# Kernel tuning notes

Measured on AMD Instinct MI355X. Metric: run time of the kernel, lower is better.

Reference implementation:

```python
import jax, jax.numpy as jnp
import numpy as np

NV, P, C, H, O = 50000, 32, 4, 64, 128
EPS = 1e-5


def _bn(x, g, b, m, v):
    # inference-mode BatchNorm1d over channel dim
    return (x - m) * jax.lax.rsqrt(v + EPS) * g + b


def setup_inputs() -> dict:
    key = jax.random.key(0)
    ks = jax.random.split(key, 16)
    voxel_features = jax.random.normal(ks[0], (NV, P, C), jnp.float32)
    voxel_num_points = jax.random.randint(ks[1], (NV,), 1, P + 1).astype(jnp.int64)
    def lin(k, fin, fout):
        kw, kb = jax.random.split(k)
        s = 1.0 / np.sqrt(fin)
        W = jax.random.uniform(kw, (fin, fout), jnp.float32, -s, s)
        b = jax.random.uniform(kb, (fout,), jnp.float32, -s, s)
        return W, b
    W1, b1 = lin(ks[2], C, H)
    W2, b2 = lin(ks[3], H, H)
    W3, b3 = lin(ks[4], H, O)
    g1 = jax.random.uniform(ks[5], (H,), jnp.float32, 0.5, 1.5)
    be1 = jax.random.normal(ks[6], (H,), jnp.float32) * 0.1
    m1 = jax.random.normal(ks[7], (H,), jnp.float32) * 0.1
    v1 = jax.random.uniform(ks[8], (H,), jnp.float32, 0.5, 1.5)
    g2 = jax.random.uniform(ks[9], (H,), jnp.float32, 0.5, 1.5)
    be2 = jax.random.normal(ks[10], (H,), jnp.float32) * 0.1
    m2 = jax.random.normal(ks[11], (H,), jnp.float32) * 0.1
    v2 = jax.random.uniform(ks[12], (H,), jnp.float32, 0.5, 1.5)
    return dict(voxel_features=voxel_features, voxel_num_points=voxel_num_points,
                W1=W1, b1=b1, g1=g1, be1=be1, m1=m1, v1=v1,
                W2=W2, b2=b2, g2=g2, be2=be2, m2=m2, v2=v2,
                W3=W3, b3=b3)


def reference(voxel_features, voxel_num_points,
              W1, b1, g1, be1, m1, v1,
              W2, b2, g2, be2, m2, v2,
              W3, b3):
    nv, p, c = voxel_features.shape
    x = voxel_features.reshape(-1, c)                 # (NV*P, C)
    x = jax.nn.relu(_bn(x @ W1 + b1, g1, be1, m1, v1))
    x = jax.nn.relu(_bn(x @ W2 + b2, g2, be2, m2, v2))
    x = x @ W3 + b3                                   # (NV*P, O)
    x = x.reshape(nv, p, -1)
    mask = jnp.arange(p)[None, :] < voxel_num_points[:, None]  # (NV, P)
    # original multiplies by mask then masked-fills -inf; net effect is -inf fill
    x = jnp.where(mask[:, :, None], x, -jnp.inf)
    return jnp.max(x, axis=1)                         # (NV, O)
```

## Files before the change

kernel.cpp:

```cpp
#include <hip/hip_runtime.h>
#include <math.h>

#define NVOX 50000
#define PPTS 32
#define HDIM 64
#define ODIM 128
#define EPSBN 1e-5f

typedef _Float16 f16x8 __attribute__((ext_vector_type(8)));
typedef _Float16 f16x4 __attribute__((ext_vector_type(4)));
typedef float f32x4 __attribute__((ext_vector_type(4)));

#define LO4(v) __builtin_shufflevector(v, v, 0, 1, 2, 3)
#define HI4(v) __builtin_shufflevector(v, v, 4, 5, 6, 7)

#define WS_W1C 0
#define WS_W2T 512
#define WS_W3T 4608
#define WS_F32_BYTE 25600
#define FOLD_THREADS 12992

__global__ void vfe_fold(
    const float* __restrict__ W1, const float* __restrict__ b1,
    const float* __restrict__ g1, const float* __restrict__ be1,
    const float* __restrict__ m1, const float* __restrict__ v1,
    const float* __restrict__ W2, const float* __restrict__ b2,
    const float* __restrict__ g2, const float* __restrict__ be2,
    const float* __restrict__ m2, const float* __restrict__ v2,
    const float* __restrict__ W3, const float* __restrict__ b3,
    _Float16* __restrict__ wsh, float* __restrict__ wsf)
{
    int t = blockIdx.x * 256 + threadIdx.x;
    if (t < 512) {
        int row = t >> 3, i = t & 7;
        float s1 = g1[row] * rsqrtf(v1[row] + EPSBN);
        float val;
        if (i < 4)      val = W1[i * 64 + row] * s1;
        else if (i == 4) val = (b1[row] - m1[row]) * s1 + be1[row];
        else             val = 0.f;
        wsh[WS_W1C + t] = (_Float16)val;
    } else if (t < 4608) {
        int e = t - 512;
        int chp = e >> 6;
        int rem = e & 63;
        int qq = rem >> 4, kc = (rem >> 2) & 3, j = rem & 3;
        int ch = kc * 16 + qq * 4 + j;
        float s2 = g2[chp] * rsqrtf(v2[chp] + EPSBN);
        wsh[t] = (_Float16)(W2[ch * 64 + chp] * s2);
    } else if (t < 12800) {
        int e = t - 4608;
        int o = e >> 6;
        int rem = e & 63;
        int php = rem >> 3, j8 = rem & 7;
        int gl = php ^ (o & 7);
        int idx = gl * 8 + j8;
        int qq = idx >> 4, kc = (idx >> 2) & 3, j = idx & 3;
        int ch = kc * 16 + qq * 4 + j;
        wsh[t] = (_Float16)W3[ch * 128 + o];
    } else if (t < 12864) {
        int i = t - 12800;
        float s2 = g2[i] * rsqrtf(v2[i] + EPSBN);
        wsf[i] = (b2[i] - m2[i]) * s2 + be2[i];
    } else if (t < FOLD_THREADS) {
        int i = t - 12864;
        wsf[64 + i] = b3[i];
    }
}

static __device__ __forceinline__ f16x4 relu4(f32x4 a) {
    f16x4 h;
    h[0] = (_Float16)fmaxf(a[0], 0.f);
    h[1] = (_Float16)fmaxf(a[1], 0.f);
    h[2] = (_Float16)fmaxf(a[2], 0.f);
    h[3] = (_Float16)fmaxf(a[3], 0.f);
    return h;
}

__global__ __launch_bounds__(256, 3) void vfe_mfma(
    const float* __restrict__ vf, const int* __restrict__ vnp,
    const _Float16* __restrict__ wsh, const float* __restrict__ wsf,
    float* __restrict__ out)
{
    __shared__ __align__(16) _Float16 sW3[ODIM * HDIM];

    const int tid  = threadIdx.x;
    const int wave = tid >> 6;
    const int lane = tid & 63;
    const int q    = lane >> 4;
    const int m16  = lane & 15;
    (void)wave;

    const int wavebase = blockIdx.x * 256 + (tid >> 6) * 64;
    const int voxA = wavebase >> 5;

    {
        const f16x8* src = (const f16x8*)&wsh[WS_W3T];
        f16x8* dst = (f16x8*)sW3;
#pragma unroll
        for (int i = 0; i < 4; ++i) dst[tid + 256 * i] = src[tid + 256 * i];
    }

    const int nA = vnp[voxA];
    const int nB = vnp[voxA + 1];

    f16x4 a1[4];
#pragma unroll
    for (int mt = 0; mt < 4; ++mt)
        a1[mt] = (q < 2) ? *(const f16x4*)&wsh[WS_W1C + (16 * mt + m16) * 8 + q * 4]
                         : (f16x4)0;
    f16x8 a2p[4][2];
#pragma unroll
    for (int mt = 0; mt < 4; ++mt)
#pragma unroll
        for (int h = 0; h < 2; ++h)
            a2p[mt][h] = *(const f16x8*)&wsh[WS_W2T + (16 * mt + m16) * 64 + q * 16 + h * 8];
    f32x4 c2v[4];
#pragma unroll
    for (int mt = 0; mt < 4; ++mt)
        c2v[mt] = *(const f32x4*)(wsf + mt * 16 + q * 4);
    float b3r[8];
#pragma unroll
    for (int nt = 0; nt < 8; ++nt) b3r[nt] = wsf[64 + nt * 16 + m16];

    float4 xv[4];
#pragma unroll
    for (int g = 0; g < 4; ++g)
        xv[g] = *(const float4*)(vf + ((size_t)wavebase + g * 16 + m16) * 4);

    f16x4 bf[4];
#pragma unroll
    for (int g = 0; g < 4; ++g) {
        f16x4 b = (f16x4)0;
        if (q == 0) {
            b[0] = (_Float16)xv[g].x; b[1] = (_Float16)xv[g].y;
            b[2] = (_Float16)xv[g].z; b[3] = (_Float16)xv[g].w;
        } else if (q == 1) {
            b[0] = (_Float16)1.0f;
        }
        bf[g] = b;
    }

    __syncthreads();

    f16x4 d1[4][4];
#pragma unroll
    for (int g = 0; g < 4; ++g)
#pragma unroll
        for (int mt = 0; mt < 4; ++mt) {
            f32x4 acc = {0.f, 0.f, 0.f, 0.f};
            acc = __builtin_amdgcn_mfma_f32_16x16x16f16(a1[mt], bf[g], acc, 0, 0, 0);
            d1[g][mt] = relu4(acc);
        }

    f16x4 d2[4][4];
#pragma unroll
    for (int g = 0; g < 4; ++g)
#pragma unroll
        for (int mt = 0; mt < 4; ++mt) {
            f32x4 acc = c2v[mt];
            acc = __builtin_amdgcn_mfma_f32_16x16x16f16(LO4(a2p[mt][0]), d1[g][0], acc, 0, 0, 0);
            acc = __builtin_amdgcn_mfma_f32_16x16x16f16(HI4(a2p[mt][0]), d1[g][1], acc, 0, 0, 0);
            acc = __builtin_amdgcn_mfma_f32_16x16x16f16(LO4(a2p[mt][1]), d1[g][2], acc, 0, 0, 0);
            acc = __builtin_amdgcn_mfma_f32_16x16x16f16(HI4(a2p[mt][1]), d1[g][3], acc, 0, 0, 0);
            d2[g][mt] = relu4(acc);
        }

    f32x4 macc4[4];
#pragma unroll
    for (int g = 0; g < 4; ++g) {
        const int n = (g < 2) ? nA : nB;
        const int slotbase = (g & 1) * 16 + q * 4;
#pragma unroll
        for (int r = 0; r < 4; ++r)
            macc4[g][r] = (slotbase + r < n) ? 0.f : -INFINITY;
    }

    float vmA[8], vmB[8];
#pragma unroll
    for (int nt = 0; nt < 8; ++nt) { vmA[nt] = -INFINITY; vmB[nt] = -INFINITY; }

#pragma unroll
    for (int nt = 0; nt < 8; ++nt) {
        const int o = nt * 16 + m16;
        f16x8 p0 = *(const f16x8*)&sW3[o * 64 + ((2 * q + 0) ^ (m16 & 7)) * 8];
        f16x8 p1 = *(const f16x8*)&sW3[o * 64 + ((2 * q + 1) ^ (m16 & 7)) * 8];
#pragma unroll
        for (int g = 0; g < 4; ++g) {
            f32x4 acc = macc4[g];
            acc = __builtin_amdgcn_mfma_f32_16x16x16f16(d2[g][0], LO4(p0), acc, 0, 0, 0);
            acc = __builtin_amdgcn_mfma_f32_16x16x16f16(d2[g][1], HI4(p0), acc, 0, 0, 0);
            acc = __builtin_amdgcn_mfma_f32_16x16x16f16(d2[g][2], LO4(p1), acc, 0, 0, 0);
            acc = __builtin_amdgcn_mfma_f32_16x16x16f16(d2[g][3], HI4(p1), acc, 0, 0, 0);
            float m0 = fmaxf(fmaxf(acc[0], acc[1]), fmaxf(acc[2], acc[3]));
            if (g < 2) vmA[nt] = fmaxf(vmA[nt], m0);
            else       vmB[nt] = fmaxf(vmB[nt], m0);
        }
    }

#pragma unroll
    for (int nt = 0; nt < 8; ++nt) {
        float t0 = vmA[nt];
        t0 = fmaxf(t0, __shfl_xor(t0, 16));
        t0 = fmaxf(t0, __shfl_xor(t0, 32));
        float t1 = vmB[nt];
        t1 = fmaxf(t1, __shfl_xor(t1, 16));
        t1 = fmaxf(t1, __shfl_xor(t1, 32));
        if (q == 0) out[(size_t)(voxA + 0) * ODIM + nt * 16 + m16] = t0 + b3r[nt];
        if (q == 1) out[(size_t)(voxA + 1) * ODIM + nt * 16 + m16] = t1 + b3r[nt];
    }
}

extern "C" void kernel_launch(void* const* d_in, const int* in_sizes, int n_in,
                              void* d_out, int out_size, void* d_ws, size_t ws_size,
                              hipStream_t stream) {
    const float* vf  = (const float*)d_in[0];
    const int*   vnp = (const int*)d_in[1];
    const float* W1  = (const float*)d_in[2];
    const float* b1  = (const float*)d_in[3];
    const float* g1  = (const float*)d_in[4];
    const float* be1 = (const float*)d_in[5];
    const float* m1  = (const float*)d_in[6];
    const float* v1  = (const float*)d_in[7];
    const float* W2  = (const float*)d_in[8];
    const float* b2  = (const float*)d_in[9];
    const float* g2  = (const float*)d_in[10];
    const float* be2 = (const float*)d_in[11];
    const float* m2  = (const float*)d_in[12];
    const float* v2  = (const float*)d_in[13];
    const float* W3  = (const float*)d_in[14];
    const float* b3  = (const float*)d_in[15];
    float* out = (float*)d_out;

    _Float16* wsh = (_Float16*)d_ws;
    float*    wsf = (float*)((char*)d_ws + WS_F32_BYTE);

    vfe_fold<<<(FOLD_THREADS + 255) / 256, 256, 0, stream>>>(
        W1, b1, g1, be1, m1, v1, W2, b2, g2, be2, m2, v2, W3, b3, wsh, wsf);

    const int blocks = (NVOX * PPTS) / 256;
    vfe_mfma<<<blocks, 256, 0, stream>>>(vf, vnp, wsh, wsf, out);
}
```

Baseline: 168.3 us.

## Process one voxel per wave, use packed f16 conversion, raise occupancy bound

Each wave now handles one voxel (32 points) instead of two, which halves the per-wave register arrays for the intermediate activations and accumulators. The launch bound is raised to 4 blocks per CU, and the grid doubles to NVOX/4 blocks. ReLU-to-f16 conversion now uses packed round-toward-zero conversion instructions instead of four scalar casts. The trade-off is that each block still copies the full W3 tile into LDS and loads all per-wave weights, so that fixed cost is paid twice as often per voxel. The conversion rounding also changes from round-to-nearest to round-toward-zero.

```diff
diff --git a/kernel.cpp b/kernel.cpp
--- a/kernel.cpp
+++ b/kernel.cpp
@@ -9,6 +9,7 @@
 
 typedef _Float16 f16x8 __attribute__((ext_vector_type(8)));
 typedef _Float16 f16x4 __attribute__((ext_vector_type(4)));
+typedef _Float16 f16x2 __attribute__((ext_vector_type(2)));
 typedef float f32x4 __attribute__((ext_vector_type(4)));
 
 #define LO4(v) __builtin_shufflevector(v, v, 0, 1, 2, 3)
@@ -68,15 +69,14 @@
 }
 
 static __device__ __forceinline__ f16x4 relu4(f32x4 a) {
-    f16x4 h;
-    h[0] = (_Float16)fmaxf(a[0], 0.f);
-    h[1] = (_Float16)fmaxf(a[1], 0.f);
-    h[2] = (_Float16)fmaxf(a[2], 0.f);
-    h[3] = (_Float16)fmaxf(a[3], 0.f);
-    return h;
-}
-
-__global__ __launch_bounds__(256, 3) void vfe_mfma(
+    f16x2 lo = __builtin_bit_cast(f16x2,
+        __builtin_amdgcn_cvt_pkrtz(fmaxf(a[0], 0.f), fmaxf(a[1], 0.f)));
+    f16x2 hi = __builtin_bit_cast(f16x2,
+        __builtin_amdgcn_cvt_pkrtz(fmaxf(a[2], 0.f), fmaxf(a[3], 0.f)));
+    return __builtin_shufflevector(lo, hi, 0, 1, 2, 3);
+}
+
+__global__ __launch_bounds__(256, 4) void vfe_mfma(
     const float* __restrict__ vf, const int* __restrict__ vnp,
     const _Float16* __restrict__ wsh, const float* __restrict__ wsf,
     float* __restrict__ out)
@@ -84,14 +84,11 @@
     __shared__ __align__(16) _Float16 sW3[ODIM * HDIM];
 
     const int tid  = threadIdx.x;
-    const int wave = tid >> 6;
     const int lane = tid & 63;
     const int q    = lane >> 4;
     const int m16  = lane & 15;
-    (void)wave;
-
-    const int wavebase = blockIdx.x * 256 + (tid >> 6) * 64;
-    const int voxA = wavebase >> 5;
+
+    const int vox = blockIdx.x * 4 + (tid >> 6);
 
     {
         const f16x8* src = (const f16x8*)&wsh[WS_W3T];
@@ -100,8 +97,7 @@
         for (int i = 0; i < 4; ++i) dst[tid + 256 * i] = src[tid + 256 * i];
     }
 
-    const int nA = vnp[voxA];
-    const int nB = vnp[voxA + 1];
+    const int n = vnp[vox];
 
     f16x4 a1[4];
 #pragma unroll
@@ -122,14 +118,14 @@
 #pragma unroll
     for (int nt = 0; nt < 8; ++nt) b3r[nt] = wsf[64 + nt * 16 + m16];
 
-    float4 xv[4];
-#pragma unroll
-    for (int g = 0; g < 4; ++g)
-        xv[g] = *(const float4*)(vf + ((size_t)wavebase + g * 16 + m16) * 4);
-
-    f16x4 bf[4];
-#pragma unroll
-    for (int g = 0; g < 4; ++g) {
+    float4 xv[2];
+#pragma unroll
+    for (int g = 0; g < 2; ++g)
+        xv[g] = *(const float4*)(vf + ((size_t)vox * 32 + g * 16 + m16) * 4);
+
+    f16x4 bf[2];
+#pragma unroll
+    for (int g = 0; g < 2; ++g) {
         f16x4 b = (f16x4)0;
         if (q == 0) {
             b[0] = (_Float16)xv[g].x; b[1] = (_Float16)xv[g].y;
@@ -142,9 +138,9 @@
 
     __syncthreads();
 
-    f16x4 d1[4][4];
-#pragma unroll
-    for (int g = 0; g < 4; ++g)
+    f16x4 d1[2][4];
+#pragma unroll
+    for (int g = 0; g < 2; ++g)
 #pragma unroll
         for (int mt = 0; mt < 4; ++mt) {
             f32x4 acc = {0.f, 0.f, 0.f, 0.f};
@@ -152,9 +148,9 @@
             d1[g][mt] = relu4(acc);
         }
 
-    f16x4 d2[4][4];
-#pragma unroll
-    for (int g = 0; g < 4; ++g)
+    f16x4 d2[2][4];
+#pragma unroll
+    for (int g = 0; g < 2; ++g)
 #pragma unroll
         for (int mt = 0; mt < 4; ++mt) {
             f32x4 acc = c2v[mt];
@@ -165,19 +161,18 @@
             d2[g][mt] = relu4(acc);
         }
 
-    f32x4 macc4[4];
-#pragma unroll
-    for (int g = 0; g < 4; ++g) {
-        const int n = (g < 2) ? nA : nB;
-        const int slotbase = (g & 1) * 16 + q * 4;
+    f32x4 macc2[2];
+#pragma unroll
+    for (int g = 0; g < 2; ++g) {
+        const int slotbase = g * 16 + q * 4;
 #pragma unroll
         for (int r = 0; r < 4; ++r)
-            macc4[g][r] = (slotbase + r < n) ? 0.f : -INFINITY;
-    }
-
-    float vmA[8], vmB[8];
-#pragma unroll
-    for (int nt = 0; nt < 8; ++nt) { vmA[nt] = -INFINITY; vmB[nt] = -INFINITY; }
+            macc2[g][r] = (slotbase + r < n) ? 0.f : -INFINITY;
+    }
+
+    float vm[8];
+#pragma unroll
+    for (int nt = 0; nt < 8; ++nt) vm[nt] = -INFINITY;
 
 #pragma unroll
     for (int nt = 0; nt < 8; ++nt) {
@@ -185,28 +180,23 @@
         f16x8 p0 = *(const f16x8*)&sW3[o * 64 + ((2 * q + 0) ^ (m16 & 7)) * 8];
         f16x8 p1 = *(const f16x8*)&sW3[o * 64 + ((2 * q + 1) ^ (m16 & 7)) * 8];
 #pragma unroll
-        for (int g = 0; g < 4; ++g) {
-            f32x4 acc = macc4[g];
+        for (int g = 0; g < 2; ++g) {
+            f32x4 acc = macc2[g];
             acc = __builtin_amdgcn_mfma_f32_16x16x16f16(d2[g][0], LO4(p0), acc, 0, 0, 0);
             acc = __builtin_amdgcn_mfma_f32_16x16x16f16(d2[g][1], HI4(p0), acc, 0, 0, 0);
             acc = __builtin_amdgcn_mfma_f32_16x16x16f16(d2[g][2], LO4(p1), acc, 0, 0, 0);
             acc = __builtin_amdgcn_mfma_f32_16x16x16f16(d2[g][3], HI4(p1), acc, 0, 0, 0);
             float m0 = fmaxf(fmaxf(acc[0], acc[1]), fmaxf(acc[2], acc[3]));
-            if (g < 2) vmA[nt] = fmaxf(vmA[nt], m0);
-            else       vmB[nt] = fmaxf(vmB[nt], m0);
+            vm[nt] = fmaxf(vm[nt], m0);
         }
     }
 
 #pragma unroll
     for (int nt = 0; nt < 8; ++nt) {
-        float t0 = vmA[nt];
+        float t0 = vm[nt];
         t0 = fmaxf(t0, __shfl_xor(t0, 16));
         t0 = fmaxf(t0, __shfl_xor(t0, 32));
-        float t1 = vmB[nt];
-        t1 = fmaxf(t1, __shfl_xor(t1, 16));
-        t1 = fmaxf(t1, __shfl_xor(t1, 32));
-        if (q == 0) out[(size_t)(voxA + 0) * ODIM + nt * 16 + m16] = t0 + b3r[nt];
-        if (q == 1) out[(size_t)(voxA + 1) * ODIM + nt * 16 + m16] = t1 + b3r[nt];
+        if (q == 0) out[(size_t)vox * ODIM + nt * 16 + m16] = t0 + b3r[nt];
     }
 }
 
@@ -237,6 +227,6 @@
     vfe_fold<<<(FOLD_THREADS + 255) / 256, 256, 0, stream>>>(
         W1, b1, g1, be1, m1, v1, W2, b2, g2, be2, m2, v2, W3, b3, wsh, wsf);
 
-    const int blocks = (NVOX * PPTS) / 256;
+    const int blocks = NVOX / 4;
     vfe_mfma<<<blocks, 256, 0, stream>>>(vf, vnp, wsh, wsf, out);
 }
```

Result: slower. 172.2 us (+2.3%).
